# Optimization experiments

Measured on AMD Instinct MI355X. Metric: run time of the kernel, lower is better.

## Reference

```python
import jax, jax.numpy as jnp
import numpy as np


def setup_inputs() -> dict:
    key = jax.random.key(0)
    ks = jax.random.split(key, 6)
    B, Q, K = 4, 512, 1024
    Dq, Dk, Dv, H = 512, 512, 512, 128
    return {
        "queries": jax.random.normal(ks[0], (B, Q, Dq), dtype=jnp.float32),
        "keys": jax.random.normal(ks[1], (B, K, Dk), dtype=jnp.float32),
        "values": jax.random.normal(ks[2], (B, K, Dv), dtype=jnp.float32),
        "W_q": jax.random.normal(ks[3], (Dq, H), dtype=jnp.float32) / np.sqrt(Dq),
        "W_k": jax.random.normal(ks[4], (Dk, H), dtype=jnp.float32) / np.sqrt(Dk),
        "w_v": jax.random.normal(ks[5], (H,), dtype=jnp.float32) / np.sqrt(H),
    }


def reference(queries, keys, values, W_q, W_k, w_v):
    # Additive (Bahdanau) attention.
    q = jnp.einsum("bqd,dh->bqh", queries, W_q)          # [B,Q,H]
    k = jnp.einsum("bkd,dh->bkh", keys, W_k)             # [B,K,H]
    features = jnp.tanh(q[:, :, None, :] + k[:, None, :, :])  # [B,Q,K,H]
    scores = jnp.einsum("bqkh,h->bqk", features, w_v)    # [B,Q,K]
    attn = jax.nn.softmax(scores, axis=-1)               # [B,Q,K]
    return jnp.einsum("bqk,bkv->bqv", attn, values)      # [B,Q,Dv]
```

## Files before the change

kernel.cpp:

```cpp
#include <hip/hip_runtime.h>

#define BB   4
#define QS   512
#define KSZ  1024
#define DD   512
#define HH   128
#define DVV  512

typedef unsigned int uint;
typedef unsigned short ushort;
typedef unsigned long long ull;
typedef __attribute__((ext_vector_type(8)))  short short8;
typedef __attribute__((ext_vector_type(16))) float f32x16;

__device__ __forceinline__ float rcp_fast(float x)  { return __builtin_amdgcn_rcpf(x); }
__device__ __forceinline__ float exp2_fast(float x) { return __builtin_amdgcn_exp2f(x); }

__device__ __forceinline__ void split1(float v, ushort& h, ushort& l) {
    uint u = __float_as_uint(v);
    h = (ushort)(u >> 16);
    float r = v - __uint_as_float(u & 0xffff0000u);
    l = (ushort)(__float_as_uint(r) >> 16);
}

#define NSQ  (BB * QS * DD / 4 / 256)
#define NSK  (BB * KSZ * DD / 4 / 256)
#define NWT  128
#define NPJ  192
#define NVT  (BB * (KSZ / 32) * (DVV / 32))

__global__ __launch_bounds__(256) void split_kernel(
    const float* __restrict__ q, const float* __restrict__ k,
    const float* __restrict__ Wq, const float* __restrict__ Wk,
    ushort* __restrict__ qh, ushort* __restrict__ ql,
    ushort* __restrict__ kh, ushort* __restrict__ kl,
    ushort* __restrict__ wqh, ushort* __restrict__ wql,
    ushort* __restrict__ wkh, ushort* __restrict__ wkl)
{
    const int id  = blockIdx.x;
    const int tid = threadIdx.x;

    if (id < NSQ + NSK) {
        const float* src; ushort* dh; ushort* dl; size_t i;
        if (id < NSQ) { src = q; dh = qh; dl = ql; i = (size_t)id * 256 + tid; }
        else          { src = k; dh = kh; dl = kl; i = (size_t)(id - NSQ) * 256 + tid; }
        float4 v = ((const float4*)src)[i];
        ushort h0,h1,h2,h3,l0,l1,l2,l3;
        split1(v.x,h0,l0); split1(v.y,h1,l1); split1(v.z,h2,l2); split1(v.w,h3,l3);
        *(ushort4*)&dh[i * 4] = make_ushort4(h0,h1,h2,h3);
        *(ushort4*)&dl[i * 4] = make_ushort4(l0,l1,l2,l3);
        return;
    }
    __shared__ float Ts[32][33];
    int t = id - (NSQ + NSK);
    const float* W; ushort* dh; ushort* dl;
    if (t < 64) { W = Wq; dh = wqh; dl = wql; }
    else        { W = Wk; dh = wkh; dl = wkl; t -= 64; }
    const int d0 = (t >> 2) * 32, h0 = (t & 3) * 32;
    {
        const int dd = tid >> 3, c4 = (tid & 7) * 4;
        float4 v = *(const float4*)&W[(size_t)(d0 + dd) * HH + h0 + c4];
        Ts[dd][c4 + 0] = v.x; Ts[dd][c4 + 1] = v.y;
        Ts[dd][c4 + 2] = v.z; Ts[dd][c4 + 3] = v.w;
    }
    __syncthreads();
    {
        const int hh = tid >> 3, d4 = (tid & 7) * 4;
        ushort h[4], l[4];
        #pragma unroll
        for (int i = 0; i < 4; i++) split1(Ts[d4 + i][hh], h[i], l[i]);
        size_t o = (size_t)(h0 + hh) * DD + d0 + d4;
        *(ushort4*)&dh[o] = make_ushort4(h[0], h[1], h[2], h[3]);
        *(ushort4*)&dl[o] = make_ushort4(l[0], l[1], l[2], l[3]);
    }
}

__global__ __launch_bounds__(256) void projvt_kernel(
    const ushort* __restrict__ qh, const ushort* __restrict__ ql,
    const ushort* __restrict__ kh, const ushort* __restrict__ kl,
    const ushort* __restrict__ wqh, const ushort* __restrict__ wql,
    const ushort* __restrict__ wkh, const ushort* __restrict__ wkl,
    const float* __restrict__ val,
    float* __restrict__ eq, float* __restrict__ ek,
    ushort* __restrict__ vhi, ushort* __restrict__ vlo)
{
    const int id  = blockIdx.x;
    const int tid = threadIdx.x;

    if (id >= NPJ) {
        __shared__ float Ts[32][33];
        const int t   = id - NPJ;
        const int b   = t >> 9;
        const int rem = t & 511;
        const int k0  = (rem >> 4) * 32;
        const int n0  = (rem & 15) * 32;
        {
            const int kk = tid >> 3, n4 = (tid & 7) * 4;
            float4 v = *(const float4*)&val[((size_t)b * KSZ + k0 + kk) * DVV + n0 + n4];
            Ts[kk][n4 + 0] = v.x; Ts[kk][n4 + 1] = v.y;
            Ts[kk][n4 + 2] = v.z; Ts[kk][n4 + 3] = v.w;
        }
        __syncthreads();
        {
            const int nn = tid >> 3, k4 = (tid & 7) * 4;
            ushort h[4], l[4];
            #pragma unroll
            for (int i = 0; i < 4; i++) split1(Ts[k4 + i][nn], h[i], l[i]);
            size_t o = ((size_t)b * DVV + n0 + nn) * KSZ + k0 + k4;
            *(ushort4*)&vhi[o] = make_ushort4(h[0], h[1], h[2], h[3]);
            *(ushort4*)&vlo[o] = make_ushort4(l[0], l[1], l[2], l[3]);
        }
        return;
    }

    const int w = tid >> 6, lane = tid & 63;
    const int row = lane & 31, kg = lane >> 5;
    const int gw = id * 4 + w;

    const ushort *pa_h, *pa_l, *pb_h, *pb_l; float* op; int m0, nt;
    if (gw < 256) {
        m0 = (gw >> 2) * 32; nt = gw & 3;
        pa_h = qh; pa_l = ql; pb_h = wqh; pb_l = wql; op = eq;
    } else {
        const int g = gw - 256;
        m0 = (g >> 2) * 32; nt = g & 3;
        pa_h = kh; pa_l = kl; pb_h = wkh; pb_l = wkl; op = ek;
    }

    const ushort* ah_p = pa_h + (size_t)(m0 + row) * DD + kg * 8;
    const ushort* al_p = pa_l + (size_t)(m0 + row) * DD + kg * 8;
    const ushort* bh_p = pb_h + (size_t)(nt * 32 + row) * DD + kg * 8;
    const ushort* bl_p = pb_l + (size_t)(nt * 32 + row) * DD + kg * 8;

    f32x16 acc;
    #pragma unroll
    for (int i = 0; i < 16; i++) acc[i] = 0.f;

    #pragma unroll 8
    for (int ks = 0; ks < DD; ks += 16) {
        short8 ah = *(const short8*)(ah_p + ks);
        short8 al = *(const short8*)(al_p + ks);
        short8 bh = *(const short8*)(bh_p + ks);
        short8 bl = *(const short8*)(bl_p + ks);
        acc = __builtin_amdgcn_mfma_f32_32x32x16_bf16(ah, bh, acc, 0, 0, 0);
        acc = __builtin_amdgcn_mfma_f32_32x32x16_bf16(ah, bl, acc, 0, 0, 0);
        acc = __builtin_amdgcn_mfma_f32_32x32x16_bf16(al, bh, acc, 0, 0, 0);
    }

    const float C2L = 2.8853900817779268f;
    float* ob = op + (size_t)m0 * HH + nt * 32;
    #pragma unroll
    for (int r = 0; r < 16; r++) {
        const int rb = (r & 3) + 8 * (r >> 2) + 4 * kg;
        ob[(size_t)rb * HH + row] = exp2_fast(acc[r] * C2L);
    }
}

__global__ __launch_bounds__(256) void scores_kernel(
    const float* __restrict__ eq, const float* __restrict__ ek,
    const float* __restrict__ wv, ushort* __restrict__ Phi,
    ushort* __restrict__ Plo, float* __restrict__ rsp)
{
    __shared__ float eqs[64][68];
    __shared__ float eks[32][68];

    const int tid = threadIdx.x;
    const int b  = blockIdx.z;
    const int q0 = blockIdx.y * 64;
    const int k0 = blockIdx.x * 32;

    const float* eqb = eq + ((size_t)b * QS  + q0) * HH;
    const float* ekb = ek + ((size_t)b * KSZ + k0) * HH;

    const int tk = tid & 15;
    const int tq = tid >> 4;

    float acc[4][2] = {};

    for (int hc = 0; hc < HH; hc += 64) {
        __syncthreads();
        #pragma unroll
        for (int i = 0; i < 4; i++) {
            int f = tid + i * 256;
            int row = f >> 4, c4 = f & 15;
            *(float4*)&eqs[row][c4 * 4] =
                *(const float4*)&eqb[(size_t)row * HH + hc + c4 * 4];
        }
        #pragma unroll
        for (int i = 0; i < 2; i++) {
            int f = tid + i * 256;
            int row = f >> 4, c4 = f & 15;
            *(float4*)&eks[row][c4 * 4] =
                *(const float4*)&ekb[(size_t)row * HH + hc + c4 * 4];
        }
        __syncthreads();

        for (int h0 = 0; h0 < 64; h0 += 4) {
            float4 wv4 = *(const float4*)&wv[hc + h0];
            float4 eq4[4], ek4[2];
            #pragma unroll
            for (int j = 0; j < 4; j++) eq4[j] = *(const float4*)&eqs[tq + 16 * j][h0];
            #pragma unroll
            for (int j = 0; j < 2; j++) ek4[j] = *(const float4*)&eks[tk + 16 * j][h0];
            #pragma unroll
            for (int jq = 0; jq < 4; jq++) {
                #pragma unroll
                for (int jk = 0; jk < 2; jk++) {
                    float u0 = fminf(fmaf(eq4[jq].x, ek4[jk].x, 1.0f), 3e7f);
                    float u1 = fminf(fmaf(eq4[jq].y, ek4[jk].y, 1.0f), 3e7f);
                    float u2 = fminf(fmaf(eq4[jq].z, ek4[jk].z, 1.0f), 3e7f);
                    float u3 = fminf(fmaf(eq4[jq].w, ek4[jk].w, 1.0f), 3e7f);
                    float p01 = u0 * u1, p23 = u2 * u3;
                    float n01 = fmaf(wv4.x, u1, wv4.y * u0);
                    float n23 = fmaf(wv4.z, u3, wv4.w * u2);
                    float N = fmaf(n01, p23, n23 * p01);
                    acc[jq][jk] = fmaf(N, rcp_fast(p01 * p23), acc[jq][jk]);
                }
            }
        }
    }

    const float CN = -2.8853900817779268f;
    ushort* ph = Phi + ((size_t)b * QS + q0) * KSZ + k0;
    ushort* pl = Plo + ((size_t)b * QS + q0) * KSZ + k0;
    #pragma unroll
    for (int jq = 0; jq < 4; jq++) {
        float rowp = 0.f;
        #pragma unroll
        for (int jk = 0; jk < 2; jk++) {
            float pv_ = exp2_fast(acc[jq][jk] * CN);
            ushort hh, ll; split1(pv_, hh, ll);
            size_t o = (size_t)(tq + 16 * jq) * KSZ + tk + 16 * jk;
            ph[o] = hh; pl[o] = ll;
            rowp += pv_;
        }
        #pragma unroll
        for (int m = 8; m; m >>= 1) rowp += __shfl_xor(rowp, m);
        if ((tid & 15) == 0)
            rsp[((size_t)b * QS + q0 + tq + 16 * jq) * 32 + blockIdx.x] = rowp;
    }
}

__global__ __launch_bounds__(256) void pv_mfma_kernel(
    const ushort* __restrict__ Phi, const ushort* __restrict__ Plo,
    const ushort* __restrict__ vhi, const ushort* __restrict__ vlo,
    const float* __restrict__ rsp, float* __restrict__ outp)
{
    __shared__ ushort PhS[64][68];
    __shared__ ushort PlS[64][68];
    __shared__ ushort VhS[64][68];
    __shared__ ushort VlS[64][68];
    __shared__ float invs[64];

    const int id  = blockIdx.x;
    const int x   = id & 7;
    const int g   = id >> 3;
    const int bmg = x * 4 + (g >> 3);
    const int b   = bmg >> 3, mt = bmg & 7;
    const int ntB = g & 7;

    const int tid = threadIdx.x, w = tid >> 6, lane = tid & 63;
    const int col = lane & 31, kg = lane >> 5;

    if (tid < 64) {
        const float* rp = rsp + ((size_t)b * QS + mt * 64 + tid) * 32;
        float s = 0.f;
        #pragma unroll
        for (int i = 0; i < 8; i++) {
            float4 v = *(const float4*)(rp + i * 4);
            s += v.x + v.y + v.z + v.w;
        }
        invs[tid] = rcp_fast(s);
    }

    const int wm = (w & 1) * 32, wn = (w >> 1) * 32;

    const int sr = tid >> 2, cc = (tid & 3) * 16;
    const ushort* gPh = Phi + ((size_t)b * QS  + mt * 64 + sr) * KSZ + cc;
    const ushort* gPl = Plo + ((size_t)b * QS  + mt * 64 + sr) * KSZ + cc;
    const ushort* gVh = vhi + ((size_t)b * DVV + ntB * 64 + sr) * KSZ + cc;
    const ushort* gVl = vlo + ((size_t)b * DVV + ntB * 64 + sr) * KSZ + cc;

    f32x16 acc;
    #pragma unroll
    for (int i = 0; i < 16; i++) acc[i] = 0.f;

    uint4 rph0, rph1, rpl0, rpl1, rvh0, rvh1, rvl0, rvl1;
#define LOADC(kc) \
    rph0 = *(const uint4*)(gPh + (kc)); rph1 = *(const uint4*)(gPh + (kc) + 8); \
    rpl0 = *(const uint4*)(gPl + (kc)); rpl1 = *(const uint4*)(gPl + (kc) + 8); \
    rvh0 = *(const uint4*)(gVh + (kc)); rvh1 = *(const uint4*)(gVh + (kc) + 8); \
    rvl0 = *(const uint4*)(gVl + (kc)); rvl1 = *(const uint4*)(gVl + (kc) + 8);
#define STOREC() { \
    ull* dPh = (ull*)&PhS[sr][cc]; ull* dPl = (ull*)&PlS[sr][cc]; \
    ull* dVh = (ull*)&VhS[sr][cc]; ull* dVl = (ull*)&VlS[sr][cc]; \
    dPh[0] = ((ull*)&rph0)[0]; dPh[1] = ((ull*)&rph0)[1]; \
    dPh[2] = ((ull*)&rph1)[0]; dPh[3] = ((ull*)&rph1)[1]; \
    dPl[0] = ((ull*)&rpl0)[0]; dPl[1] = ((ull*)&rpl0)[1]; \
    dPl[2] = ((ull*)&rpl1)[0]; dPl[3] = ((ull*)&rpl1)[1]; \
    dVh[0] = ((ull*)&rvh0)[0]; dVh[1] = ((ull*)&rvh0)[1]; \
    dVh[2] = ((ull*)&rvh1)[0]; dVh[3] = ((ull*)&rvh1)[1]; \
    dVl[0] = ((ull*)&rvl0)[0]; dVl[1] = ((ull*)&rvl0)[1]; \
    dVl[2] = ((ull*)&rvl1)[0]; dVl[3] = ((ull*)&rvl1)[1]; }

    LOADC(0);
    STOREC();
    __syncthreads();

    for (int c = 0; c < 16; c++) {
        if (c < 15) { LOADC((c + 1) * 64); }
        #pragma unroll
        for (int kk = 0; kk < 4; kk++) {
            const int off = kk * 16 + kg * 8;
            short8 ah, al, vh, vl;
            { const ull* p = (const ull*)&PhS[wm + col][off];
              ((ull*)&ah)[0] = p[0]; ((ull*)&ah)[1] = p[1]; }
            { const ull* p = (const ull*)&PlS[wm + col][off];
              ((ull*)&al)[0] = p[0]; ((ull*)&al)[1] = p[1]; }
            { const ull* p = (const ull*)&VhS[wn + col][off];
              ((ull*)&vh)[0] = p[0]; ((ull*)&vh)[1] = p[1]; }
            { const ull* p = (const ull*)&VlS[wn + col][off];
              ((ull*)&vl)[0] = p[0]; ((ull*)&vl)[1] = p[1]; }
            acc = __builtin_amdgcn_mfma_f32_32x32x16_bf16(ah, vh, acc, 0, 0, 0);
            acc = __builtin_amdgcn_mfma_f32_32x32x16_bf16(ah, vl, acc, 0, 0, 0);
            acc = __builtin_amdgcn_mfma_f32_32x32x16_bf16(al, vh, acc, 0, 0, 0);
        }
        __syncthreads();
        if (c < 15) { STOREC(); __syncthreads(); }
    }

    float* ob = outp + ((size_t)b * QS + mt * 64 + wm) * DVV + ntB * 64 + wn;
    #pragma unroll
    for (int r = 0; r < 16; r++) {
        const int rb = (r & 3) + 8 * (r >> 2) + 4 * kg;
        ob[(size_t)rb * DVV + col] = acc[r] * invs[wm + rb];
    }
#undef LOADC
#undef STOREC
}

extern "C" void kernel_launch(void* const* d_in, const int* in_sizes, int n_in,
                              void* d_out, int out_size, void* d_ws, size_t ws_size,
                              hipStream_t stream)
{
    const float* queries = (const float*)d_in[0];
    const float* keys    = (const float*)d_in[1];
    const float* values  = (const float*)d_in[2];
    const float* Wq      = (const float*)d_in[3];
    const float* Wk      = (const float*)d_in[4];
    const float* wv      = (const float*)d_in[5];
    float* out = (float*)d_out;

    float*  eq  = (float*)d_ws;
    float*  ek  = eq + (size_t)BB * QS * HH;
    float*  rsp = ek + (size_t)BB * KSZ * HH;
    ushort* Phi = (ushort*)(rsp + (size_t)BB * QS * 32);
    ushort* Plo = Phi + (size_t)BB * QS * KSZ;
    ushort* vhi = Plo + (size_t)BB * QS * KSZ;
    ushort* vlo = vhi + (size_t)BB * KSZ * DVV;
    ushort* qh  = vlo + (size_t)BB * KSZ * DVV;
    ushort* ql  = qh  + (size_t)BB * QS * DD;
    ushort* kh  = ql  + (size_t)BB * QS * DD;
    ushort* kl  = kh  + (size_t)BB * KSZ * DD;
    ushort* wqh = kl  + (size_t)BB * KSZ * DD;
    ushort* wql = wqh + (size_t)HH * DD;
    ushort* wkh = wql + (size_t)HH * DD;
    ushort* wkl = wkh + (size_t)HH * DD;

    split_kernel<<<dim3(NSQ + NSK + NWT), 256, 0, stream>>>(
        queries, keys, Wq, Wk, qh, ql, kh, kl, wqh, wql, wkh, wkl);

    projvt_kernel<<<dim3(NPJ + NVT), 256, 0, stream>>>(
        qh, ql, kh, kl, wqh, wql, wkh, wkl, values, eq, ek, vhi, vlo);

    scores_kernel<<<dim3(KSZ / 32, QS / 64, BB), 256, 0, stream>>>(
        eq, ek, wv, Phi, Plo, rsp);

    pv_mfma_kernel<<<dim3(256), 256, 0, stream>>>(Phi, Plo, vhi, vlo, rsp, out);
}
```

Before: 146.3 us.

## Fuse score computation and PV matmul into one split-K kernel with normalize pass

Combines the scores kernel and the PV MFMA kernel into a single kernel. Each block computes a 64x32 tile of exp-scores in shared memory and immediately multiplies it against V fragments loaded from global memory, so the bf16 hi/lo P matrices no longer go through HBM. The key dimension is split across 8 blocks. Partial outputs and row sums are written to a workspace and reduced by a new normalize kernel. In exchange it adds 8x partial-output traffic, for about 32MB of writes and reads. Grid parallelism for the score computation also drops to 256 blocks of 512 threads, and each block recomputes per k-slice with less register tiling.

```diff
diff --git a/kernel.cpp b/kernel.cpp
--- a/kernel.cpp
+++ b/kernel.cpp
@@ -156,187 +156,186 @@
     }
 }
 
-__global__ __launch_bounds__(256) void scores_kernel(
+__global__ __launch_bounds__(512, 2) void spv_kernel(
     const float* __restrict__ eq, const float* __restrict__ ek,
-    const float* __restrict__ wv, ushort* __restrict__ Phi,
-    ushort* __restrict__ Plo, float* __restrict__ rsp)
-{
-    __shared__ float eqs[64][68];
-    __shared__ float eks[32][68];
-
-    const int tid = threadIdx.x;
-    const int b  = blockIdx.z;
-    const int q0 = blockIdx.y * 64;
-    const int k0 = blockIdx.x * 32;
-
-    const float* eqb = eq + ((size_t)b * QS  + q0) * HH;
-    const float* ekb = ek + ((size_t)b * KSZ + k0) * HH;
-
-    const int tk = tid & 15;
-    const int tq = tid >> 4;
-
-    float acc[4][2] = {};
-
-    for (int hc = 0; hc < HH; hc += 64) {
+    const float* __restrict__ wv,
+    const ushort* __restrict__ vhi, const ushort* __restrict__ vlo,
+    float* __restrict__ opart, float* __restrict__ rsp)
+{
+    __shared__ float  eqs[64][132];
+    __shared__ float  eks[32][132];
+    __shared__ ushort PhS[64][36];
+    __shared__ ushort PlS[64][36];
+
+    const int id  = blockIdx.x;
+    const int bk  = id & 31;
+    const int qt  = id >> 5;
+    const int b   = bk >> 3;
+    const int kp  = bk & 7;
+
+    const int tid  = threadIdx.x;
+    const int w    = tid >> 6, lane = tid & 63;
+    const int col  = lane & 31, kg = lane >> 5;
+    const int wq   = (w & 1) * 32;
+    const int wn   = (w >> 1) * 128;
+    const int tq   = tid >> 4;
+    const int tk   = tid & 15;
+
+    const float* eqg = eq + ((size_t)b * QS + qt * 64) * HH;
+    #pragma unroll
+    for (int i = 0; i < 4; i++) {
+        int f = tid + i * 512;
+        int row = f >> 5, c4 = (f & 31) * 4;
+        *(float4*)&eqs[row][c4] = *(const float4*)&eqg[(size_t)row * HH + c4];
+    }
+    const float* ekg = ek + ((size_t)b * KSZ + kp * 128) * HH;
+    #pragma unroll
+    for (int i = 0; i < 2; i++) {
+        int f = tid + i * 512;
+        int row = f >> 5, c4 = (f & 31) * 4;
+        *(float4*)&eks[row][c4] = *(const float4*)&ekg[(size_t)row * HH + c4];
+    }
+    __syncthreads();
+
+    f32x16 acc[4];
+    #pragma unroll
+    for (int n = 0; n < 4; n++) {
+        #pragma unroll
+        for (int i = 0; i < 16; i++) acc[n][i] = 0.f;
+    }
+    float rowacc0 = 0.f, rowacc1 = 0.f;
+
+    const size_t vrow0 = ((size_t)b * DVV + wn + col) * KSZ + kp * 128;
+    const ushort* vh_p = vhi + vrow0;
+    const ushort* vl_p = vlo + vrow0;
+
+#define SGROUP(eqv, ekv, sacc) { \
+    float u0 = fminf(fmaf((eqv).x, (ekv).x, 1.0f), 3e7f); \
+    float u1 = fminf(fmaf((eqv).y, (ekv).y, 1.0f), 3e7f); \
+    float u2 = fminf(fmaf((eqv).z, (ekv).z, 1.0f), 3e7f); \
+    float u3 = fminf(fmaf((eqv).w, (ekv).w, 1.0f), 3e7f); \
+    float p01 = u0 * u1, p23 = u2 * u3; \
+    float n01 = fmaf(wv4.x, u1, wv4.y * u0); \
+    float n23 = fmaf(wv4.z, u3, wv4.w * u2); \
+    float Nn = fmaf(n01, p23, n23 * p01); \
+    sacc = fmaf(Nn, rcp_fast(p01 * p23), sacc); }
+
+    for (int s = 0; s < 4; s++) {
+        uint4 bhf[8], blf[8];
+        #pragma unroll
+        for (int nb = 0; nb < 4; nb++) {
+            #pragma unroll
+            for (int k2 = 0; k2 < 2; k2++) {
+                const size_t o = (size_t)(nb * 32) * KSZ + s * 32 + k2 * 16 + kg * 8;
+                bhf[nb * 2 + k2] = *(const uint4*)(vh_p + o);
+                blf[nb * 2 + k2] = *(const uint4*)(vl_p + o);
+            }
+        }
+        float4 eknxt0, eknxt1;
+        if (s < 3) {
+            int f0 = tid, f1 = tid + 512;
+            eknxt0 = *(const float4*)&ekg[(size_t)((s + 1) * 32 + (f0 >> 5)) * HH + (f0 & 31) * 4];
+            eknxt1 = *(const float4*)&ekg[(size_t)((s + 1) * 32 + (f1 >> 5)) * HH + (f1 & 31) * 4];
+        }
+
+        float s00 = 0.f, s01 = 0.f, s10 = 0.f, s11 = 0.f;
+        #pragma unroll 2
+        for (int h = 0; h < HH; h += 4) {
+            float4 wv4 = *(const float4*)&wv[h];
+            float4 eqa = *(const float4*)&eqs[tq][h];
+            float4 eqb = *(const float4*)&eqs[tq + 32][h];
+            float4 eka = *(const float4*)&eks[tk][h];
+            float4 ekb = *(const float4*)&eks[tk + 16][h];
+            SGROUP(eqa, eka, s00);
+            SGROUP(eqa, ekb, s01);
+            SGROUP(eqb, eka, s10);
+            SGROUP(eqb, ekb, s11);
+        }
+        {
+            const float CN = -2.8853900817779268f;
+            float p00 = exp2_fast(s00 * CN);
+            float p01v = exp2_fast(s01 * CN);
+            float p10 = exp2_fast(s10 * CN);
+            float p11 = exp2_fast(s11 * CN);
+            ushort hh, ll;
+            split1(p00,  hh, ll); PhS[tq][tk]           = hh; PlS[tq][tk]           = ll;
+            split1(p01v, hh, ll); PhS[tq][tk + 16]      = hh; PlS[tq][tk + 16]      = ll;
+            split1(p10,  hh, ll); PhS[tq + 32][tk]      = hh; PlS[tq + 32][tk]      = ll;
+            split1(p11,  hh, ll); PhS[tq + 32][tk + 16] = hh; PlS[tq + 32][tk + 16] = ll;
+            rowacc0 += p00 + p01v;
+            rowacc1 += p10 + p11;
+        }
         __syncthreads();
-        #pragma unroll
-        for (int i = 0; i < 4; i++) {
-            int f = tid + i * 256;
-            int row = f >> 4, c4 = f & 15;
-            *(float4*)&eqs[row][c4 * 4] =
-                *(const float4*)&eqb[(size_t)row * HH + hc + c4 * 4];
-        }
-        #pragma unroll
-        for (int i = 0; i < 2; i++) {
-            int f = tid + i * 256;
-            int row = f >> 4, c4 = f & 15;
-            *(float4*)&eks[row][c4 * 4] =
-                *(const float4*)&ekb[(size_t)row * HH + hc + c4 * 4];
+
+        if (s < 3) {
+            int f0 = tid, f1 = tid + 512;
+            *(float4*)&eks[f0 >> 5][(f0 & 31) * 4] = eknxt0;
+            *(float4*)&eks[f1 >> 5][(f1 & 31) * 4] = eknxt1;
+        }
+
+        #pragma unroll
+        for (int k2 = 0; k2 < 2; k2++) {
+            short8 ah, al;
+            { const ull* p = (const ull*)&PhS[wq + col][k2 * 16 + kg * 8];
+              ((ull*)&ah)[0] = p[0]; ((ull*)&ah)[1] = p[1]; }
+            { const ull* p = (const ull*)&PlS[wq + col][k2 * 16 + kg * 8];
+              ((ull*)&al)[0] = p[0]; ((ull*)&al)[1] = p[1]; }
+            #pragma unroll
+            for (int nb = 0; nb < 4; nb++) {
+                short8 vh = *(const short8*)&bhf[nb * 2 + k2];
+                short8 vl = *(const short8*)&blf[nb * 2 + k2];
+                acc[nb] = __builtin_amdgcn_mfma_f32_32x32x16_bf16(ah, vh, acc[nb], 0, 0, 0);
+                acc[nb] = __builtin_amdgcn_mfma_f32_32x32x16_bf16(ah, vl, acc[nb], 0, 0, 0);
+                acc[nb] = __builtin_amdgcn_mfma_f32_32x32x16_bf16(al, vh, acc[nb], 0, 0, 0);
+            }
         }
         __syncthreads();
-
-        for (int h0 = 0; h0 < 64; h0 += 4) {
-            float4 wv4 = *(const float4*)&wv[hc + h0];
-            float4 eq4[4], ek4[2];
-            #pragma unroll
-            for (int j = 0; j < 4; j++) eq4[j] = *(const float4*)&eqs[tq + 16 * j][h0];
-            #pragma unroll
-            for (int j = 0; j < 2; j++) ek4[j] = *(const float4*)&eks[tk + 16 * j][h0];
-            #pragma unroll
-            for (int jq = 0; jq < 4; jq++) {
-                #pragma unroll
-                for (int jk = 0; jk < 2; jk++) {
-                    float u0 = fminf(fmaf(eq4[jq].x, ek4[jk].x, 1.0f), 3e7f);
-                    float u1 = fminf(fmaf(eq4[jq].y, ek4[jk].y, 1.0f), 3e7f);
-                    float u2 = fminf(fmaf(eq4[jq].z, ek4[jk].z, 1.0f), 3e7f);
-                    float u3 = fminf(fmaf(eq4[jq].w, ek4[jk].w, 1.0f), 3e7f);
-                    float p01 = u0 * u1, p23 = u2 * u3;
-                    float n01 = fmaf(wv4.x, u1, wv4.y * u0);
-                    float n23 = fmaf(wv4.z, u3, wv4.w * u2);
-                    float N = fmaf(n01, p23, n23 * p01);
-                    acc[jq][jk] = fmaf(N, rcp_fast(p01 * p23), acc[jq][jk]);
-                }
-            }
-        }
-    }
-
-    const float CN = -2.8853900817779268f;
-    ushort* ph = Phi + ((size_t)b * QS + q0) * KSZ + k0;
-    ushort* pl = Plo + ((size_t)b * QS + q0) * KSZ + k0;
-    #pragma unroll
-    for (int jq = 0; jq < 4; jq++) {
-        float rowp = 0.f;
-        #pragma unroll
-        for (int jk = 0; jk < 2; jk++) {
-            float pv_ = exp2_fast(acc[jq][jk] * CN);
-            ushort hh, ll; split1(pv_, hh, ll);
-            size_t o = (size_t)(tq + 16 * jq) * KSZ + tk + 16 * jk;
-            ph[o] = hh; pl[o] = ll;
-            rowp += pv_;
-        }
-        #pragma unroll
-        for (int m = 8; m; m >>= 1) rowp += __shfl_xor(rowp, m);
-        if ((tid & 15) == 0)
-            rsp[((size_t)b * QS + q0 + tq + 16 * jq) * 32 + blockIdx.x] = rowp;
-    }
-}
-
-__global__ __launch_bounds__(256) void pv_mfma_kernel(
-    const ushort* __restrict__ Phi, const ushort* __restrict__ Plo,
-    const ushort* __restrict__ vhi, const ushort* __restrict__ vlo,
-    const float* __restrict__ rsp, float* __restrict__ outp)
-{
-    __shared__ ushort PhS[64][68];
-    __shared__ ushort PlS[64][68];
-    __shared__ ushort VhS[64][68];
-    __shared__ ushort VlS[64][68];
-    __shared__ float invs[64];
-
-    const int id  = blockIdx.x;
-    const int x   = id & 7;
-    const int g   = id >> 3;
-    const int bmg = x * 4 + (g >> 3);
-    const int b   = bmg >> 3, mt = bmg & 7;
-    const int ntB = g & 7;
-
-    const int tid = threadIdx.x, w = tid >> 6, lane = tid & 63;
-    const int col = lane & 31, kg = lane >> 5;
-
-    if (tid < 64) {
-        const float* rp = rsp + ((size_t)b * QS + mt * 64 + tid) * 32;
-        float s = 0.f;
-        #pragma unroll
-        for (int i = 0; i < 8; i++) {
-            float4 v = *(const float4*)(rp + i * 4);
-            s += v.x + v.y + v.z + v.w;
-        }
-        invs[tid] = rcp_fast(s);
-    }
-
-    const int wm = (w & 1) * 32, wn = (w >> 1) * 32;
-
-    const int sr = tid >> 2, cc = (tid & 3) * 16;
-    const ushort* gPh = Phi + ((size_t)b * QS  + mt * 64 + sr) * KSZ + cc;
-    const ushort* gPl = Plo + ((size_t)b * QS  + mt * 64 + sr) * KSZ + cc;
-    const ushort* gVh = vhi + ((size_t)b * DVV + ntB * 64 + sr) * KSZ + cc;
-    const ushort* gVl = vlo + ((size_t)b * DVV + ntB * 64 + sr) * KSZ + cc;
-
-    f32x16 acc;
-    #pragma unroll
-    for (int i = 0; i < 16; i++) acc[i] = 0.f;
-
-    uint4 rph0, rph1, rpl0, rpl1, rvh0, rvh1, rvl0, rvl1;
-#define LOADC(kc) \
-    rph0 = *(const uint4*)(gPh + (kc)); rph1 = *(const uint4*)(gPh + (kc) + 8); \
-    rpl0 = *(const uint4*)(gPl + (kc)); rpl1 = *(const uint4*)(gPl + (kc) + 8); \
-    rvh0 = *(const uint4*)(gVh + (kc)); rvh1 = *(const uint4*)(gVh + (kc) + 8); \
-    rvl0 = *(const uint4*)(gVl + (kc)); rvl1 = *(const uint4*)(gVl + (kc) + 8);
-#define STOREC() { \
-    ull* dPh = (ull*)&PhS[sr][cc]; ull* dPl = (ull*)&PlS[sr][cc]; \
-    ull* dVh = (ull*)&VhS[sr][cc]; ull* dVl = (ull*)&VlS[sr][cc]; \
-    dPh[0] = ((ull*)&rph0)[0]; dPh[1] = ((ull*)&rph0)[1]; \
-    dPh[2] = ((ull*)&rph1)[0]; dPh[3] = ((ull*)&rph1)[1]; \
-    dPl[0] = ((ull*)&rpl0)[0]; dPl[1] = ((ull*)&rpl0)[1]; \
-    dPl[2] = ((ull*)&rpl1)[0]; dPl[3] = ((ull*)&rpl1)[1]; \
-    dVh[0] = ((ull*)&rvh0)[0]; dVh[1] = ((ull*)&rvh0)[1]; \
-    dVh[2] = ((ull*)&rvh1)[0]; dVh[3] = ((ull*)&rvh1)[1]; \
-    dVl[0] = ((ull*)&rvl0)[0]; dVl[1] = ((ull*)&rvl0)[1]; \
-    dVl[2] = ((ull*)&rvl1)[0]; dVl[3] = ((ull*)&rvl1)[1]; }
-
-    LOADC(0);
-    STOREC();
-    __syncthreads();
-
-    for (int c = 0; c < 16; c++) {
-        if (c < 15) { LOADC((c + 1) * 64); }
-        #pragma unroll
-        for (int kk = 0; kk < 4; kk++) {
-            const int off = kk * 16 + kg * 8;
-            short8 ah, al, vh, vl;
-            { const ull* p = (const ull*)&PhS[wm + col][off];
-              ((ull*)&ah)[0] = p[0]; ((ull*)&ah)[1] = p[1]; }
-            { const ull* p = (const ull*)&PlS[wm + col][off];
-              ((ull*)&al)[0] = p[0]; ((ull*)&al)[1] = p[1]; }
-            { const ull* p = (const ull*)&VhS[wn + col][off];
-              ((ull*)&vh)[0] = p[0]; ((ull*)&vh)[1] = p[1]; }
-            { const ull* p = (const ull*)&VlS[wn + col][off];
-              ((ull*)&vl)[0] = p[0]; ((ull*)&vl)[1] = p[1]; }
-            acc = __builtin_amdgcn_mfma_f32_32x32x16_bf16(ah, vh, acc, 0, 0, 0);
-            acc = __builtin_amdgcn_mfma_f32_32x32x16_bf16(ah, vl, acc, 0, 0, 0);
-            acc = __builtin_amdgcn_mfma_f32_32x32x16_bf16(al, vh, acc, 0, 0, 0);
-        }
-        __syncthreads();
-        if (c < 15) { STOREC(); __syncthreads(); }
-    }
-
-    float* ob = outp + ((size_t)b * QS + mt * 64 + wm) * DVV + ntB * 64 + wn;
-    #pragma unroll
-    for (int r = 0; r < 16; r++) {
-        const int rb = (r & 3) + 8 * (r >> 2) + 4 * kg;
-        ob[(size_t)rb * DVV + col] = acc[r] * invs[wm + rb];
-    }
-#undef LOADC
-#undef STOREC
+    }
+#undef SGROUP
+
+    #pragma unroll
+    for (int m = 8; m; m >>= 1) {
+        rowacc0 += __shfl_xor(rowacc0, m);
+        rowacc1 += __shfl_xor(rowacc1, m);
+    }
+    if (tk == 0) {
+        rsp[((size_t)b * QS + qt * 64 + tq) * 8 + kp]      = rowacc0;
+        rsp[((size_t)b * QS + qt * 64 + tq + 32) * 8 + kp] = rowacc1;
+    }
+
+    float* ob = opart + (((size_t)kp * BB + b) * QS + qt * 64 + wq) * DVV + wn;
+    #pragma unroll
+    for (int nb = 0; nb < 4; nb++) {
+        #pragma unroll
+        for (int r = 0; r < 16; r++) {
+            const int rb = (r & 3) + 8 * (r >> 2) + 4 * kg;
+            ob[(size_t)rb * DVV + nb * 32 + col] = acc[nb][r];
+        }
+    }
+}
+
+__global__ __launch_bounds__(256) void norm_kernel(
+    const float* __restrict__ opart, const float* __restrict__ rsp,
+    float* __restrict__ outp)
+{
+    const int i  = blockIdx.x * 256 + threadIdx.x;
+    const int n4 = (i & 127) * 4;
+    const int q  = (i >> 7) & (QS - 1);
+    const int b  = i >> 16;
+
+    const float* rp = rsp + ((size_t)b * QS + q) * 8;
+    float4 r0 = *(const float4*)rp;
+    float4 r1 = *(const float4*)(rp + 4);
+    float inv = rcp_fast(r0.x + r0.y + r0.z + r0.w + r1.x + r1.y + r1.z + r1.w);
+
+    float ox = 0.f, oy = 0.f, oz = 0.f, ow = 0.f;
+    #pragma unroll
+    for (int kp = 0; kp < 8; kp++) {
+        float4 v = *(const float4*)&opart[(((size_t)kp * BB + b) * QS + q) * DVV + n4];
+        ox += v.x; oy += v.y; oz += v.z; ow += v.w;
+    }
+    float4 res = make_float4(ox * inv, oy * inv, oz * inv, ow * inv);
+    *(float4*)&outp[((size_t)b * QS + q) * DVV + n4] = res;
 }
 
 extern "C" void kernel_launch(void* const* d_in, const int* in_sizes, int n_in,
@@ -351,12 +350,11 @@
     const float* wv      = (const float*)d_in[5];
     float* out = (float*)d_out;
 
-    float*  eq  = (float*)d_ws;
-    float*  ek  = eq + (size_t)BB * QS * HH;
-    float*  rsp = ek + (size_t)BB * KSZ * HH;
-    ushort* Phi = (ushort*)(rsp + (size_t)BB * QS * 32);
-    ushort* Plo = Phi + (size_t)BB * QS * KSZ;
-    ushort* vhi = Plo + (size_t)BB * QS * KSZ;
+    float*  eq    = (float*)d_ws;
+    float*  ek    = eq  + (size_t)BB * QS * HH;
+    float*  rsp   = ek  + (size_t)BB * KSZ * HH;
+    float*  opart = rsp + (size_t)BB * QS * 8;
+    ushort* vhi = (ushort*)(opart + (size_t)8 * BB * QS * DVV);
     ushort* vlo = vhi + (size_t)BB * KSZ * DVV;
     ushort* qh  = vlo + (size_t)BB * KSZ * DVV;
     ushort* ql  = qh  + (size_t)BB * QS * DD;
@@ -373,8 +371,7 @@
     projvt_kernel<<<dim3(NPJ + NVT), 256, 0, stream>>>(
         qh, ql, kh, kl, wqh, wql, wkh, wkl, values, eq, ek, vhi, vlo);
 
-    scores_kernel<<<dim3(KSZ / 32, QS / 64, BB), 256, 0, stream>>>(
-        eq, ek, wv, Phi, Plo, rsp);
-
-    pv_mfma_kernel<<<dim3(256), 256, 0, stream>>>(Phi, Plo, vhi, vlo, rsp, out);
-}
+    spv_kernel<<<dim3(256), 512, 0, stream>>>(eq, ek, wv, vhi, vlo, opart, rsp);
+
+    norm_kernel<<<dim3(1024), 256, 0, stream>>>(opart, rsp, out);
+}
```

New measurement: 152.3 us. 4.1% more time.
